# Optimization experiments

Measured on AMD Instinct MI355X. Metric: run time of the kernel, lower is better.

Reference implementation:

```python
import jax, jax.numpy as jnp
import numpy as np

B, N, C, W = 128, 512, 128, 128
MASK_FILL = -1e-06  # faithful to original (sic: -1e-06, not -1e6)


def setup_inputs() -> dict:
    key = jax.random.key(0)
    ks = jax.random.split(key, 8)
    s = 1.0 / np.sqrt(C)
    return {
        "x": jax.random.normal(ks[0], (B, N, C), dtype=jnp.float32),
        "Wq": jax.random.normal(ks[1], (C, W), dtype=jnp.float32) * s,
        "bq": jnp.zeros((W,), dtype=jnp.float32),
        "Wk": jax.random.normal(ks[2], (C, W), dtype=jnp.float32) * s,
        "bk": jnp.zeros((W,), dtype=jnp.float32),
        "Wv": jax.random.normal(ks[3], (C, W), dtype=jnp.float32) * s,
        "bv": jnp.zeros((W,), dtype=jnp.float32),
        "valid_len": jax.random.randint(ks[4], (B,), 0, N, dtype=jnp.int64),
    }


def reference(x, Wq, bq, Wk, bk, Wv, bv, valid_len):
    # QKV projections: [B, N, W]
    q = jnp.einsum("bnc,cw->bnw", x, Wq) + bq
    k = jnp.einsum("bnc,cw->bnw", x, Wk) + bk
    v = jnp.einsum("bnc,cw->bnw", x, Wv) + bv
    # scores: [B, N, N]
    scores = jnp.einsum("bnw,bmw->bnm", q, k)
    # masked softmax: positions m where m > valid_len[b] get MASK_FILL
    # (mask is identical across query rows n since valid_len is per-batch)
    keep = jnp.arange(N)[None, None, :] <= valid_len[:, None, None]  # [B,1,N]
    scores = jnp.where(keep, scores, MASK_FILL)
    attn = jax.nn.softmax(scores, axis=-1)
    return jnp.einsum("bnm,bmw->bnw", attn, v)
```

## Files before the change

kernel.cpp:

```cpp
#include <hip/hip_runtime.h>
#include <hip/hip_fp16.h>
#include <math.h>

#define B_ 128
#define N_ 512
#define C_ 128
#define W_ 128
#define LDSW 136

typedef _Float16 f16;
typedef _Float16 f16x8 __attribute__((ext_vector_type(8)));
typedef _Float16 f16x4 __attribute__((ext_vector_type(4)));
typedef float f32x4 __attribute__((ext_vector_type(4)));

#define MFMA16(a, b, c) __builtin_amdgcn_mfma_f32_16x16x32_f16(a, b, c, 0, 0, 0)

#define LOG2E 1.44269504f
#define MASKF (-1e-6f * LOG2E)

__global__ __launch_bounds__(256) void prep_w(const float* __restrict__ Wq,
                                              const float* __restrict__ Wk,
                                              const float* __restrict__ Wv,
                                              f16* __restrict__ wT) {
  __shared__ float xs[128 * 129];
  const float* src = blockIdx.x == 0 ? Wq : (blockIdx.x == 1 ? Wk : Wv);
  f16* dst = wT + (size_t)blockIdx.x * C_ * W_;
  const int t = threadIdx.x;
  for (int i = 0; i < 16; ++i) {
    int idx = t + 256 * i;
    int c = idx >> 5, w4 = idx & 31;
    float4 v = *reinterpret_cast<const float4*>(src + c * W_ + w4 * 4);
    xs[c * 129 + w4 * 4 + 0] = v.x;
    xs[c * 129 + w4 * 4 + 1] = v.y;
    xs[c * 129 + w4 * 4 + 2] = v.z;
    xs[c * 129 + w4 * 4 + 3] = v.w;
  }
  __syncthreads();
  for (int i = 0; i < 64; ++i) {
    int idx = t + 256 * i;
    int w = idx >> 7, c = idx & 127;
    dst[idx] = (f16)xs[c * 129 + w];
  }
}

__global__ __launch_bounds__(256) void proj(const float* __restrict__ x,
                                            const float* __restrict__ bq,
                                            const float* __restrict__ bk,
                                            const float* __restrict__ bv,
                                            const f16* __restrict__ wT,
                                            f16* __restrict__ q,
                                            f16* __restrict__ k,
                                            f16* __restrict__ vT) {
  __shared__ f16 xs[128 * LDSW];
  __shared__ f16 wls[128 * LDSW];
  const int b = blockIdx.y, n0 = blockIdx.x * 128;
  const int t = threadIdx.x, wave = t >> 6, lane = t & 63;
  const int quad = lane >> 4, l15 = lane & 15;

  for (int i = 0; i < 16; ++i) {
    int idx = t + 256 * i;
    int row = idx >> 5, c4 = idx & 31;
    const float4 v = *reinterpret_cast<const float4*>(
        x + ((size_t)(b * N_ + n0 + row)) * C_ + c4 * 4);
    f16x4 h;
    h.x = (f16)v.x; h.y = (f16)v.y; h.z = (f16)v.z; h.w = (f16)v.w;
    *reinterpret_cast<f16x4*>(&xs[row * LDSW + c4 * 4]) = h;
  }
  __syncthreads();

  f16x8 af[2][4];
  for (int mt = 0; mt < 2; ++mt)
    for (int ks = 0; ks < 4; ++ks)
      af[mt][ks] = *reinterpret_cast<const f16x8*>(
          &xs[(wave * 32 + mt * 16 + l15) * LDSW + ks * 32 + quad * 8]);

  for (int ph = 0; ph < 3; ++ph) {
    __syncthreads();
    for (int i = 0; i < 8; ++i) {
      int idx = t + 256 * i;
      int row = idx >> 4, c16 = idx & 15;
      *reinterpret_cast<f16x8*>(&wls[row * LDSW + c16 * 8]) =
          *reinterpret_cast<const f16x8*>(wT + (size_t)ph * 16384 + idx * 8);
    }
    __syncthreads();

    f32x4 acc[2][8];
    for (int mt = 0; mt < 2; ++mt)
      for (int ct = 0; ct < 8; ++ct) acc[mt][ct] = {0.f, 0.f, 0.f, 0.f};

    for (int ct = 0; ct < 8; ++ct)
      for (int ks = 0; ks < 4; ++ks) {
        f16x8 bf = *reinterpret_cast<const f16x8*>(
            &wls[(ct * 16 + l15) * LDSW + ks * 32 + quad * 8]);
        acc[0][ct] = MFMA16(af[0][ks], bf, acc[0][ct]);
        acc[1][ct] = MFMA16(af[1][ks], bf, acc[1][ct]);
      }

    if (ph < 2) {
      const float* bias = ph == 0 ? bq : bk;
      const float scale = ph == 0 ? LOG2E : 1.0f;
      f16* dst = ph == 0 ? q : k;
      for (int mt = 0; mt < 2; ++mt)
        for (int ct = 0; ct < 8; ++ct) {
          int wcol = ct * 16 + l15;
          float bb = bias[wcol];
          for (int r = 0; r < 4; ++r) {
            int n = n0 + wave * 32 + mt * 16 + quad * 4 + r;
            dst[((size_t)(b * N_ + n)) * W_ + wcol] =
                (f16)((acc[mt][ct][r] + bb) * scale);
          }
        }
    } else {
      for (int mt = 0; mt < 2; ++mt)
        for (int ct = 0; ct < 8; ++ct) {
          int wcol = ct * 16 + l15;
          float bb = bv[wcol];
          int n = n0 + wave * 32 + mt * 16 + quad * 4;
          f16x4 h;
          h.x = (f16)(acc[mt][ct][0] + bb);
          h.y = (f16)(acc[mt][ct][1] + bb);
          h.z = (f16)(acc[mt][ct][2] + bb);
          h.w = (f16)(acc[mt][ct][3] + bb);
          *reinterpret_cast<f16x4*>(&vT[((size_t)(b * W_ + wcol)) * N_ + n]) = h;
        }
    }
  }
}

__global__ __launch_bounds__(256, 2) void flash(const f16* __restrict__ q,
                                                const f16* __restrict__ k,
                                                const f16* __restrict__ vT,
                                                const int* __restrict__ vlen,
                                                float* __restrict__ out) {
  __shared__ f16 pls[128 * LDSW];
  const int b = blockIdx.x, m0 = blockIdx.y * 128;
  const int t = threadIdx.x, wave = t >> 6, lane = t & 63;
  const int quad = lane >> 4, l15 = lane & 15;
  const int vl = vlen[b];
  const int mcol = m0 + wave * 32;

  f16x8 qf[2][4];
  for (int ct = 0; ct < 2; ++ct)
    for (int kt = 0; kt < 4; ++kt)
      qf[ct][kt] = *reinterpret_cast<const f16x8*>(
          q + ((size_t)(b * N_ + mcol + ct * 16 + l15)) * W_ + kt * 32 +
          quad * 8);

  f32x4 oacc[8][2];
  for (int wt = 0; wt < 8; ++wt)
    for (int ct = 0; ct < 2; ++ct) oacc[wt][ct] = {0.f, 0.f, 0.f, 0.f};
  float mrun[2] = {-3.4e38f, -3.4e38f}, lrun[2] = {0.f, 0.f};

  f16* prow = &pls[(size_t)wave * 32 * LDSW];

  for (int j = 0; j < 4; ++j) {
    const int n0 = j * 128;

    f32x4 sacc[8][2];
    for (int i = 0; i < 8; ++i) {
      sacc[i][0] = {0.f, 0.f, 0.f, 0.f};
      sacc[i][1] = {0.f, 0.f, 0.f, 0.f};
      f16x8 kf[4];
      for (int kt = 0; kt < 4; ++kt)
        kf[kt] = *reinterpret_cast<const f16x8*>(
            k + ((size_t)(b * N_ + n0 + 16 * i + l15)) * W_ + kt * 32 +
            quad * 8);
      for (int kt = 0; kt < 4; ++kt) {
        sacc[i][0] = MFMA16(kf[kt], qf[0][kt], sacc[i][0]);
        sacc[i][1] = MFMA16(kf[kt], qf[1][kt], sacc[i][1]);
      }
    }

    for (int i = 0; i < 8; ++i)
      for (int r = 0; r < 4; ++r) {
        int n = n0 + 16 * i + quad * 4 + r;
        if (n > vl) { sacc[i][0][r] = MASKF; sacc[i][1][r] = MASKF; }
      }

    float alpha[2];
    for (int ct = 0; ct < 2; ++ct) {
      float mx = -3.4e38f;
      for (int i = 0; i < 8; ++i)
        for (int r = 0; r < 4; ++r) mx = fmaxf(mx, sacc[i][ct][r]);
      mx = fmaxf(mx, __shfl_xor(mx, 16));
      mx = fmaxf(mx, __shfl_xor(mx, 32));
      float mnew = fmaxf(mrun[ct], mx);
      alpha[ct] = exp2f(mrun[ct] - mnew);
      mrun[ct] = mnew;
      float s = 0.f;
      for (int i = 0; i < 8; ++i)
        for (int r = 0; r < 4; ++r) {
          float p = exp2f(sacc[i][ct][r] - mnew);
          sacc[i][ct][r] = p;
          s += p;
        }
      s += __shfl_xor(s, 16);
      s += __shfl_xor(s, 32);
      lrun[ct] = lrun[ct] * alpha[ct] + s;
    }

    for (int i = 0; i < 8; ++i)
      for (int ct = 0; ct < 2; ++ct) {
        f16x4 h;
        h.x = (f16)sacc[i][ct][0];
        h.y = (f16)sacc[i][ct][1];
        h.z = (f16)sacc[i][ct][2];
        h.w = (f16)sacc[i][ct][3];
        *reinterpret_cast<f16x4*>(
            &prow[(ct * 16 + l15) * LDSW + 16 * i + quad * 4]) = h;
      }

    for (int wt = 0; wt < 8; ++wt) {
      oacc[wt][0] *= alpha[0];
      oacc[wt][1] *= alpha[1];
    }

    f16x8 pf[2][4];
    for (int ct = 0; ct < 2; ++ct)
      for (int kt = 0; kt < 4; ++kt)
        pf[ct][kt] = *reinterpret_cast<const f16x8*>(
            &prow[(ct * 16 + l15) * LDSW + kt * 32 + quad * 8]);

    for (int wt = 0; wt < 8; ++wt) {
      f16x8 vf[4];
      for (int kt = 0; kt < 4; ++kt)
        vf[kt] = *reinterpret_cast<const f16x8*>(
            vT + ((size_t)(b * W_ + 16 * wt + l15)) * N_ + n0 + kt * 32 +
            quad * 8);
      for (int kt = 0; kt < 4; ++kt) {
        oacc[wt][0] = MFMA16(vf[kt], pf[0][kt], oacc[wt][0]);
        oacc[wt][1] = MFMA16(vf[kt], pf[1][kt], oacc[wt][1]);
      }
    }
  }

  for (int ct = 0; ct < 2; ++ct) {
    float inv = 1.f / lrun[ct];
    int m = mcol + ct * 16 + l15;
    for (int wt = 0; wt < 8; ++wt) {
      int w = 16 * wt + quad * 4;
      float4 o;
      o.x = oacc[wt][ct][0] * inv;
      o.y = oacc[wt][ct][1] * inv;
      o.z = oacc[wt][ct][2] * inv;
      o.w = oacc[wt][ct][3] * inv;
      *reinterpret_cast<float4*>(&out[((size_t)(b * N_ + m)) * W_ + w]) = o;
    }
  }
}

extern "C" void kernel_launch(void* const* d_in, const int* in_sizes, int n_in,
                              void* d_out, int out_size, void* d_ws,
                              size_t ws_size, hipStream_t stream) {
  const float* x  = (const float*)d_in[0];
  const float* Wq = (const float*)d_in[1];
  const float* bq = (const float*)d_in[2];
  const float* Wk = (const float*)d_in[3];
  const float* bk = (const float*)d_in[4];
  const float* Wv = (const float*)d_in[5];
  const float* bv = (const float*)d_in[6];
  const int* vlen = (const int*)d_in[7];
  float* out = (float*)d_out;

  char* ws = (char*)d_ws;
  f16* wT = (f16*)ws;
  f16* q  = (f16*)(ws + (1u << 20));
  f16* k  = (f16*)(ws + (1u << 20) + (16u << 20));
  f16* vT = (f16*)(ws + (1u << 20) + (32u << 20));

  prep_w<<<3, 256, 0, stream>>>(Wq, Wk, Wv, wT);
  proj<<<dim3(4, 128), 256, 0, stream>>>(x, bq, bk, bv, wT, q, k, vT);
  flash<<<dim3(128, 4), 256, 0, stream>>>(q, k, vT, vlen, out);
}
```

Measured before the change: 172.5 us.

## Split flash PV across waves by output column, stage K in LDS, parallelize weight prep

The flash kernel now loads each K tile into shared memory once per block instead of every wave reading it from global memory. The P·V product is repartitioned so each wave owns 32 output columns across all 128 query rows, reading the full shared P tile. Per-row rescale and normalization factors are broadcast through LDS, which adds extra block-wide barriers. prep_w now uses 24 blocks instead of 3, and proj reads weight fragments straight from global memory without LDS staging.

```diff
diff --git a/kernel.cpp b/kernel.cpp
--- a/kernel.cpp
+++ b/kernel.cpp
@@ -22,25 +22,26 @@
                                               const float* __restrict__ Wk,
                                               const float* __restrict__ Wv,
                                               f16* __restrict__ wT) {
-  __shared__ float xs[128 * 129];
+  __shared__ float xs[16 * 129];
   const float* src = blockIdx.x == 0 ? Wq : (blockIdx.x == 1 ? Wk : Wv);
   f16* dst = wT + (size_t)blockIdx.x * C_ * W_;
+  const int c0 = blockIdx.y * 16;
   const int t = threadIdx.x;
-  for (int i = 0; i < 16; ++i) {
-    int idx = t + 256 * i;
-    int c = idx >> 5, w4 = idx & 31;
-    float4 v = *reinterpret_cast<const float4*>(src + c * W_ + w4 * 4);
-    xs[c * 129 + w4 * 4 + 0] = v.x;
-    xs[c * 129 + w4 * 4 + 1] = v.y;
-    xs[c * 129 + w4 * 4 + 2] = v.z;
-    xs[c * 129 + w4 * 4 + 3] = v.w;
-  }
-  __syncthreads();
-  for (int i = 0; i < 64; ++i) {
-    int idx = t + 256 * i;
-    int w = idx >> 7, c = idx & 127;
-    dst[idx] = (f16)xs[c * 129 + w];
-  }
+  for (int ii = 0; ii < 2; ++ii) {
+    int idx = t + 256 * ii;
+    int row = idx >> 5, w4 = idx & 31;
+    float4 v = *reinterpret_cast<const float4*>(src + (c0 + row) * W_ + w4 * 4);
+    xs[row * 129 + w4 * 4 + 0] = v.x;
+    xs[row * 129 + w4 * 4 + 1] = v.y;
+    xs[row * 129 + w4 * 4 + 2] = v.z;
+    xs[row * 129 + w4 * 4 + 3] = v.w;
+  }
+  __syncthreads();
+  int o = t * 8;
+  int w = o >> 4, cc = o & 15;
+  f16x8 h;
+  for (int jj = 0; jj < 8; ++jj) h[jj] = (f16)xs[(cc + jj) * 129 + w];
+  *reinterpret_cast<f16x8*>(dst + w * C_ + c0 + cc) = h;
 }
 
 __global__ __launch_bounds__(256) void proj(const float* __restrict__ x,
@@ -52,7 +53,6 @@
                                             f16* __restrict__ k,
                                             f16* __restrict__ vT) {
   __shared__ f16 xs[128 * LDSW];
-  __shared__ f16 wls[128 * LDSW];
   const int b = blockIdx.y, n0 = blockIdx.x * 128;
   const int t = threadIdx.x, wave = t >> 6, lane = t & 63;
   const int quad = lane >> 4, l15 = lane & 15;
@@ -75,26 +75,21 @@
           &xs[(wave * 32 + mt * 16 + l15) * LDSW + ks * 32 + quad * 8]);
 
   for (int ph = 0; ph < 3; ++ph) {
-    __syncthreads();
-    for (int i = 0; i < 8; ++i) {
-      int idx = t + 256 * i;
-      int row = idx >> 4, c16 = idx & 15;
-      *reinterpret_cast<f16x8*>(&wls[row * LDSW + c16 * 8]) =
-          *reinterpret_cast<const f16x8*>(wT + (size_t)ph * 16384 + idx * 8);
-    }
-    __syncthreads();
-
     f32x4 acc[2][8];
     for (int mt = 0; mt < 2; ++mt)
       for (int ct = 0; ct < 8; ++ct) acc[mt][ct] = {0.f, 0.f, 0.f, 0.f};
 
-    for (int ct = 0; ct < 8; ++ct)
+    for (int ct = 0; ct < 8; ++ct) {
+      f16x8 wf[4];
+      for (int ks = 0; ks < 4; ++ks)
+        wf[ks] = *reinterpret_cast<const f16x8*>(
+            wT + (size_t)ph * 16384 + (ct * 16 + l15) * C_ + ks * 32 +
+            quad * 8);
       for (int ks = 0; ks < 4; ++ks) {
-        f16x8 bf = *reinterpret_cast<const f16x8*>(
-            &wls[(ct * 16 + l15) * LDSW + ks * 32 + quad * 8]);
-        acc[0][ct] = MFMA16(af[0][ks], bf, acc[0][ct]);
-        acc[1][ct] = MFMA16(af[1][ks], bf, acc[1][ct]);
-      }
+        acc[0][ct] = MFMA16(af[0][ks], wf[ks], acc[0][ct]);
+        acc[1][ct] = MFMA16(af[1][ks], wf[ks], acc[1][ct]);
+      }
+    }
 
     if (ph < 2) {
       const float* bias = ph == 0 ? bq : bk;
@@ -132,7 +127,9 @@
                                                 const f16* __restrict__ vT,
                                                 const int* __restrict__ vlen,
                                                 float* __restrict__ out) {
+  __shared__ f16 kls[128 * LDSW];
   __shared__ f16 pls[128 * LDSW];
+  __shared__ float bcast[128];
   const int b = blockIdx.x, m0 = blockIdx.y * 128;
   const int t = threadIdx.x, wave = t >> 6, lane = t & 63;
   const int quad = lane >> 4, l15 = lane & 15;
@@ -146,15 +143,22 @@
           q + ((size_t)(b * N_ + mcol + ct * 16 + l15)) * W_ + kt * 32 +
           quad * 8);
 
-  f32x4 oacc[8][2];
-  for (int wt = 0; wt < 8; ++wt)
-    for (int ct = 0; ct < 2; ++ct) oacc[wt][ct] = {0.f, 0.f, 0.f, 0.f};
+  f32x4 oacc[2][8];
+  for (int wt = 0; wt < 2; ++wt)
+    for (int cm = 0; cm < 8; ++cm) oacc[wt][cm] = {0.f, 0.f, 0.f, 0.f};
   float mrun[2] = {-3.4e38f, -3.4e38f}, lrun[2] = {0.f, 0.f};
-
-  f16* prow = &pls[(size_t)wave * 32 * LDSW];
 
   for (int j = 0; j < 4; ++j) {
     const int n0 = j * 128;
+
+    for (int i = 0; i < 8; ++i) {
+      int idx = t + 256 * i;
+      int row = idx >> 4, c16 = idx & 15;
+      f16x8 tmp = *reinterpret_cast<const f16x8*>(
+          k + ((size_t)(b * N_ + n0 + row)) * W_ + c16 * 8);
+      *reinterpret_cast<f16x8*>(&kls[row * LDSW + c16 * 8]) = tmp;
+    }
+    __syncthreads();
 
     f32x4 sacc[8][2];
     for (int i = 0; i < 8; ++i) {
@@ -163,8 +167,7 @@
       f16x8 kf[4];
       for (int kt = 0; kt < 4; ++kt)
         kf[kt] = *reinterpret_cast<const f16x8*>(
-            k + ((size_t)(b * N_ + n0 + 16 * i + l15)) * W_ + kt * 32 +
-            quad * 8);
+            &kls[(i * 16 + l15) * LDSW + kt * 32 + quad * 8]);
       for (int kt = 0; kt < 4; ++kt) {
         sacc[i][0] = MFMA16(kf[kt], qf[0][kt], sacc[i][0]);
         sacc[i][1] = MFMA16(kf[kt], qf[1][kt], sacc[i][1]);
@@ -207,43 +210,53 @@
         h.z = (f16)sacc[i][ct][2];
         h.w = (f16)sacc[i][ct][3];
         *reinterpret_cast<f16x4*>(
-            &prow[(ct * 16 + l15) * LDSW + 16 * i + quad * 4]) = h;
-      }
-
-    for (int wt = 0; wt < 8; ++wt) {
-      oacc[wt][0] *= alpha[0];
-      oacc[wt][1] *= alpha[1];
-    }
-
-    f16x8 pf[2][4];
-    for (int ct = 0; ct < 2; ++ct)
+            &pls[(wave * 32 + ct * 16 + l15) * LDSW + 16 * i + quad * 4]) = h;
+      }
+    if (quad == 0) {
+      bcast[wave * 32 + l15] = alpha[0];
+      bcast[wave * 32 + 16 + l15] = alpha[1];
+    }
+
+    f16x8 vf[2][4];
+    for (int wt = 0; wt < 2; ++wt)
       for (int kt = 0; kt < 4; ++kt)
-        pf[ct][kt] = *reinterpret_cast<const f16x8*>(
-            &prow[(ct * 16 + l15) * LDSW + kt * 32 + quad * 8]);
-
-    for (int wt = 0; wt < 8; ++wt) {
-      f16x8 vf[4];
+        vf[wt][kt] = *reinterpret_cast<const f16x8*>(
+            vT + ((size_t)(b * W_ + wave * 32 + wt * 16 + l15)) * N_ + n0 +
+            kt * 32 + quad * 8);
+    __syncthreads();
+
+    float al[8];
+    for (int cm = 0; cm < 8; ++cm) al[cm] = bcast[cm * 16 + l15];
+    for (int wt = 0; wt < 2; ++wt)
+      for (int cm = 0; cm < 8; ++cm) oacc[wt][cm] *= al[cm];
+    for (int cm = 0; cm < 8; ++cm) {
+      f16x8 pf[4];
       for (int kt = 0; kt < 4; ++kt)
-        vf[kt] = *reinterpret_cast<const f16x8*>(
-            vT + ((size_t)(b * W_ + 16 * wt + l15)) * N_ + n0 + kt * 32 +
-            quad * 8);
+        pf[kt] = *reinterpret_cast<const f16x8*>(
+            &pls[(cm * 16 + l15) * LDSW + kt * 32 + quad * 8]);
       for (int kt = 0; kt < 4; ++kt) {
-        oacc[wt][0] = MFMA16(vf[kt], pf[0][kt], oacc[wt][0]);
-        oacc[wt][1] = MFMA16(vf[kt], pf[1][kt], oacc[wt][1]);
-      }
-    }
-  }
-
-  for (int ct = 0; ct < 2; ++ct) {
-    float inv = 1.f / lrun[ct];
-    int m = mcol + ct * 16 + l15;
-    for (int wt = 0; wt < 8; ++wt) {
-      int w = 16 * wt + quad * 4;
+        oacc[0][cm] = MFMA16(vf[0][kt], pf[kt], oacc[0][cm]);
+        oacc[1][cm] = MFMA16(vf[1][kt], pf[kt], oacc[1][cm]);
+      }
+    }
+  }
+
+  __syncthreads();
+  if (quad == 0) {
+    bcast[wave * 32 + l15] = 1.f / lrun[0];
+    bcast[wave * 32 + 16 + l15] = 1.f / lrun[1];
+  }
+  __syncthreads();
+  for (int cm = 0; cm < 8; ++cm) {
+    float inv = bcast[cm * 16 + l15];
+    int m = m0 + cm * 16 + l15;
+    for (int wt = 0; wt < 2; ++wt) {
+      int w = wave * 32 + wt * 16 + quad * 4;
       float4 o;
-      o.x = oacc[wt][ct][0] * inv;
-      o.y = oacc[wt][ct][1] * inv;
-      o.z = oacc[wt][ct][2] * inv;
-      o.w = oacc[wt][ct][3] * inv;
+      o.x = oacc[wt][cm][0] * inv;
+      o.y = oacc[wt][cm][1] * inv;
+      o.z = oacc[wt][cm][2] * inv;
+      o.w = oacc[wt][cm][3] * inv;
       *reinterpret_cast<float4*>(&out[((size_t)(b * N_ + m)) * W_ + w]) = o;
     }
   }
@@ -268,7 +281,7 @@
   f16* k  = (f16*)(ws + (1u << 20) + (16u << 20));
   f16* vT = (f16*)(ws + (1u << 20) + (32u << 20));
 
-  prep_w<<<3, 256, 0, stream>>>(Wq, Wk, Wv, wT);
+  prep_w<<<dim3(3, 8), 256, 0, stream>>>(Wq, Wk, Wv, wT);
   proj<<<dim3(4, 128), 256, 0, stream>>>(x, bq, bk, bv, wT, q, k, vT);
   flash<<<dim3(128, 4), 256, 0, stream>>>(q, k, vT, vlen, out);
 }
```

After: 157.3 us. -8.8%, faster.
